# Kernel optimization log

Measured on AMD Instinct MI355X. Metric: run time of the kernel, lower is better.

Reference implementation:

```python
import jax, jax.numpy as jnp
import numpy as np
import math

N = 50000      # nodes
E = 800000     # edges
F_IN = 64      # input node features
H = 4          # heads
C = 32         # hidden_channels (per-head dim)
HC = H * C     # 128
ED = 4         # edge_dim
G = 1000       # graphs in batch


def _lin(key, fin, fout, bias=True):
    k1, k2 = jax.random.split(key)
    w = jax.random.normal(k1, (fin, fout), jnp.float32) * (1.0 / math.sqrt(fin))
    if bias:
        b = jax.random.normal(k2, (fout,), jnp.float32) * 0.02
        return w, b
    return w


def setup_inputs() -> dict:
    key = jax.random.key(0)
    ks = jax.random.split(key, 24)
    x = jax.random.normal(ks[0], (N, F_IN), jnp.float32)
    edge_index = jax.random.randint(ks[1], (2, E), 0, N)
    edge_attr = jax.random.normal(ks[2], (E, ED), jnp.float32)
    batch = jnp.sort(jax.random.randint(ks[3], (N,), 0, G))
    inp = {"x": x, "edge_index": edge_index, "edge_attr": edge_attr, "batch": batch}
    fins = [F_IN, HC, HC]
    i = 4
    for l in range(3):
        fin = fins[l]
        inp[f"wq{l+1}"], inp[f"bq{l+1}"] = _lin(ks[i], fin, HC); i += 1
        inp[f"wk{l+1}"], inp[f"bk{l+1}"] = _lin(ks[i], fin, HC); i += 1
        inp[f"wv{l+1}"], inp[f"bv{l+1}"] = _lin(ks[i], fin, HC); i += 1
        inp[f"we{l+1}"] = _lin(ks[i], ED, HC, bias=False); i += 1
        inp[f"ws{l+1}"], inp[f"bs{l+1}"] = _lin(ks[i], fin, HC); i += 1
    inp["wlin"], inp["blin"] = _lin(ks[i], HC, 1)
    return inp


def _segment_softmax(alpha, seg, n):
    # numerically-stable softmax over edges grouped by destination node
    m = jax.ops.segment_max(alpha, seg, num_segments=n)
    m = jnp.where(jnp.isfinite(m), m, 0.0)
    a = jnp.exp(alpha - m[seg])
    s = jax.ops.segment_sum(a, seg, num_segments=n)
    return a / (s[seg] + 1e-16)


def _conv(x, src, dst, ea, wq, bq, wk, bk, wv, bv, we, ws, bs):
    # PyG TransformerConv (concat=True, root_weight=True, beta=False)
    n = x.shape[0]
    q = (x @ wq + bq).reshape(n, H, C)
    k = (x @ wk + bk).reshape(n, H, C)
    v = (x @ wv + bv).reshape(n, H, C)
    e = (ea @ we).reshape(-1, H, C)          # [E,H,C] edge projection
    kj = k[src] + e                           # key of source + edge
    alpha = jnp.einsum('ehc,ehc->eh', q[dst], kj) / math.sqrt(C)  # [E,H]
    alpha = _segment_softmax(alpha, dst, n)
    msg = (v[src] + e) * alpha[..., None]     # [E,H,C]
    out = jax.ops.segment_sum(msg, dst, num_segments=n).reshape(n, HC)
    return out + x @ ws + bs                  # skip connection


def reference(x, edge_index, edge_attr, batch,
              wq1, bq1, wk1, bk1, wv1, bv1, we1, ws1, bs1,
              wq2, bq2, wk2, bk2, wv2, bv2, we2, ws2, bs2,
              wq3, bq3, wk3, bk3, wv3, bv3, we3, ws3, bs3,
              wlin, blin):
    src, dst = edge_index[0], edge_index[1]
    h = jax.nn.relu(_conv(x, src, dst, edge_attr, wq1, bq1, wk1, bk1, wv1, bv1, we1, ws1, bs1))
    h = jax.nn.relu(_conv(h, src, dst, edge_attr, wq2, bq2, wk2, bk2, wv2, bv2, we2, ws2, bs2))
    h = _conv(h, src, dst, edge_attr, wq3, bq3, wk3, bk3, wv3, bv3, we3, ws3, bs3)
    # global_mean_pool
    s = jax.ops.segment_sum(h, batch, num_segments=G)
    cnt = jax.ops.segment_sum(jnp.ones((h.shape[0],), h.dtype), batch, num_segments=G)
    pooled = s / jnp.maximum(cnt, 1.0)[:, None]
    # dropout is identity in eval mode
    return pooled @ wlin + blin
```

## Files before the change

kernel.cpp:

```cpp
#include <hip/hip_runtime.h>
#include <math.h>

#define NN 50000
#define EE 800000
#define GG 1000

typedef __attribute__((ext_vector_type(2))) _Float16 h2f;
typedef __attribute__((ext_vector_type(4))) _Float16 h4f;
typedef __attribute__((ext_vector_type(8))) _Float16 h8f;
typedef __attribute__((ext_vector_type(4))) float f32x4;

#if __has_builtin(__builtin_amdgcn_fdot2)
#define FDOT2(a, b, c) __builtin_amdgcn_fdot2((a), (b), (c), false)
#else
#define FDOT2(a, b, c) ((float)(a)[0] * (float)(b)[0] + (float)(a)[1] * (float)(b)[1] + (c))
#endif

static inline int ceil_div(int a, int b) { return (a + b - 1) / b; }

union EU { int2 i; h4f h; };


__global__ __launch_bounds__(256) void hist_k(const int* __restrict__ ei, int* __restrict__ cnt)
{
    int e = blockIdx.x * 256 + threadIdx.x;
    if (e >= EE) return;
    atomicAdd(&cnt[ei[EE + e]], 1);
}

__global__ __launch_bounds__(1024) void scan1_k(const int* __restrict__ cnt, int n,
                                                int* __restrict__ rowptr, int* __restrict__ bsum)
{
    __shared__ int tmp[1024];
    const int tid = threadIdx.x;
    const int i = blockIdx.x * 1024 + tid;
    tmp[tid] = (i < n) ? cnt[i] : 0;
    __syncthreads();
    for (int off = 1; off < 1024; off <<= 1) {
        int t = (tid >= off) ? tmp[tid - off] : 0;
        __syncthreads();
        tmp[tid] += t;
        __syncthreads();
    }
    if (i < n) rowptr[i + 1] = tmp[tid];
    if (tid == 1023) bsum[blockIdx.x] = tmp[1023];
}

__global__ __launch_bounds__(64) void scan2_k(int* __restrict__ bsum, int nb)
{
    const int t = threadIdx.x;
    int v = (t < nb) ? bsum[t] : 0;
    const int orig = v;
    for (int off = 1; off < 64; off <<= 1) {
        int n = __shfl_up(v, off);
        if (t >= off) v += n;
    }
    if (t < nb) bsum[t] = v - orig;
}

__global__ __launch_bounds__(1024) void scan3_k(int* __restrict__ rowptr,
                                                int* __restrict__ wcur,
                                                const int* __restrict__ bsum, int n)
{
    int i = blockIdx.x * 1024 + threadIdx.x;
    if (i < n) {
        int v = rowptr[i + 1] + bsum[blockIdx.x];
        rowptr[i + 1] = v;
        if (i + 1 < n) wcur[i + 1] = v;
    }
    if (i == 0) { rowptr[0] = 0; wcur[0] = 0; }
}

__global__ __launch_bounds__(256) void scatter_k(const int* __restrict__ ei,
                                                 const float4* __restrict__ ea,
                                                 int* __restrict__ wcur,
                                                 int4* __restrict__ edges)
{
    int e = blockIdx.x * 256 + threadIdx.x;
    if (e >= EE) return;
    int dst = ei[EE + e];
    int pos = atomicAdd(&wcur[dst], 1);
    float4 a = ea[e];
    EU u; u.h = h4f{(_Float16)a.x, (_Float16)a.y, (_Float16)a.z, (_Float16)a.w};
    edges[pos] = make_int4(ei[e], u.i.x, u.i.y, 0);
}

struct W12 { const float* w[12]; };

__global__ __launch_bounds__(64) void shuffle_w12(W12 ws, _Float16* __restrict__ out)
{
    const int m = blockIdx.y;
    const int K = (m < 4) ? 64 : 128;
    const int nblk = (K / 16) * 8;
    if (blockIdx.x >= nblk) return;
    const int s = blockIdx.x >> 3, c16 = blockIdx.x & 7;
    const int lane = threadIdx.x;
    const float* __restrict__ w = ws.w[m];
    const int kbase = s * 16 + (lane >> 4) * 4;
    const int col = c16 * 16 + (lane & 15);
    h4f h;
#pragma unroll
    for (int j = 0; j < 4; ++j) h[j] = (_Float16)w[(size_t)(kbase + j) * 128 + col];
    size_t base = (m < 4) ? (size_t)m * 64 * 128
                          : (size_t)4 * 64 * 128 + (size_t)(m - 4) * 128 * 128;
    reinterpret_cast<h4f*>(out + base)[(size_t)blockIdx.x * 64 + lane] = h;
}

template<int K, bool F32IN>
__global__ __launch_bounds__(256) void gemm_mfma(
    const void* __restrict__ xin, const _Float16* __restrict__ wshuf,
    const float* __restrict__ bq, const float* __restrict__ bk,
    const float* __restrict__ bv, const float* __restrict__ bs,
    _Float16* __restrict__ qout, _Float16* __restrict__ kout,
    _Float16* __restrict__ vout, float* __restrict__ skout)
{
    constexpr int KS = K / 16;
    constexpr int PADK = K + 8;
    __shared__ _Float16 xs[64 * PADK];
    __shared__ _Float16 wt[K * 128];
    const int t = threadIdx.x;
    const int bn = blockIdx.x * 64;
    if (F32IN) {
        const float* xf = (const float*)xin;
        constexpr int C4 = K / 4;
        for (int idx = t; idx < 64 * C4; idx += 256) {
            const int row = idx / C4, c4 = idx % C4;
            float4 val = make_float4(0.f, 0.f, 0.f, 0.f);
            if (bn + row < NN)
                val = reinterpret_cast<const float4*>(xf)[(size_t)(bn + row) * C4 + c4];
            h4f h = {(_Float16)val.x, (_Float16)val.y, (_Float16)val.z, (_Float16)val.w};
            *reinterpret_cast<h4f*>(&xs[row * PADK + c4 * 4]) = h;
        }
    } else {
        const _Float16* xh = (const _Float16*)xin;
        constexpr int CH = K / 8;
        for (int idx = t; idx < 64 * CH; idx += 256) {
            const int row = idx / CH, ch = idx % CH;
            h8f val = {0, 0, 0, 0, 0, 0, 0, 0};
            if (bn + row < NN)
                val = reinterpret_cast<const h8f*>(xh + (size_t)(bn + row) * K)[ch];
            *reinterpret_cast<h8f*>(&xs[row * PADK + ch * 8]) = val;
        }
    }
    __syncthreads();

    const int wid = t >> 6, lane = t & 63;
    const int rloc = wid * 16 + (lane & 15);
    const int ko = (lane >> 4) * 4;
    h4f b[KS];
#pragma unroll
    for (int s = 0; s < KS; ++s)
        b[s] = *reinterpret_cast<const h4f*>(&xs[rloc * PADK + s * 16 + ko]);

    const int node = bn + rloc;
    const int hcq = (lane >> 4) * 4;
    const float* bias[4] = {bq, bk, bv, bs};
    constexpr int WH4 = K * 128 / 4;

#pragma unroll
    for (int m = 0; m < 4; ++m) {
        const h4f* __restrict__ wg = reinterpret_cast<const h4f*>(wshuf + (size_t)m * K * 128);
        h4f* __restrict__ wl = reinterpret_cast<h4f*>(wt);
        for (int idx = t; idx < WH4; idx += 256) wl[idx] = wg[idx];
        __syncthreads();

        f32x4 acc[8];
#pragma unroll
        for (int c = 0; c < 8; ++c) acc[c] = {0, 0, 0, 0};
#pragma unroll
        for (int c = 0; c < 8; ++c)
#pragma unroll
            for (int s = 0; s < KS; ++s) {
                h4f af = wl[(s * 8 + c) * 64 + lane];
                acc[c] = __builtin_amdgcn_mfma_f32_16x16x16f16(af, b[s], acc[c], 0, 0, 0);
            }
        if (node < NN) {
            const float* bm = bias[m];
#pragma unroll
            for (int c = 0; c < 8; ++c) {
                const int hc = c * 16 + hcq;
                const float4 bb = *reinterpret_cast<const float4*>(&bm[hc]);
                float o0 = acc[c][0] + bb.x, o1 = acc[c][1] + bb.y;
                float o2 = acc[c][2] + bb.z, o3 = acc[c][3] + bb.w;
                if (m == 3) {
                    *reinterpret_cast<float4*>(&skout[(size_t)node * 128 + hc]) =
                        make_float4(o0, o1, o2, o3);
                } else {
                    _Float16* dst = (m == 0) ? qout : (m == 1) ? kout : vout;
                    h4f oh = {(_Float16)o0, (_Float16)o1, (_Float16)o2, (_Float16)o3};
                    *reinterpret_cast<h4f*>(&dst[(size_t)node * 128 + hc]) = oh;
                }
            }
        }
        __syncthreads();
    }
}

__global__ __launch_bounds__(256, 8) void node_agg(
    const int* __restrict__ rowptr, const int4* __restrict__ edges,
    const _Float16* __restrict__ qh, const _Float16* __restrict__ kh,
    const _Float16* __restrict__ vh, const float* __restrict__ we,
    const float* __restrict__ sk, _Float16* __restrict__ houth, int relu)
{
    __shared__ float we_s[4 * 128];
    const int t = threadIdx.x;
    if (t < 128)
        reinterpret_cast<float4*>(we_s)[t] = reinterpret_cast<const float4*>(we)[t];
    __syncthreads();
    const int node = blockIdx.x * 4 + (t >> 6);
    if (node >= NN) return;
    const int lane = t & 63;
    const int g = lane >> 4, sub = lane & 15, ch0 = sub * 8;
    const int beg = rowptr[node], end = rowptr[node + 1];
    const int deg = end - beg;

    const float sc = 0.17677669529663687f * 1.4426950408889634f;
    const h8f q8 = *reinterpret_cast<const h8f*>(&qh[(size_t)node * 128 + ch0]);
    float qf[8];
#pragma unroll
    for (int j = 0; j < 8; ++j) qf[j] = (float)q8[j] * sc;
    h2f qp[4];
#pragma unroll
    for (int i = 0; i < 4; ++i) {
        qp[i][0] = (_Float16)qf[2 * i];
        qp[i][1] = (_Float16)qf[2 * i + 1];
    }

    float qe[4];
#pragma unroll
    for (int d = 0; d < 4; ++d) {
        const float4 wa = *reinterpret_cast<const float4*>(&we_s[d * 128 + ch0]);
        const float4 wb = *reinterpret_cast<const float4*>(&we_s[d * 128 + ch0 + 4]);
        float pq = wa.x * qf[0] + wa.y * qf[1] + wa.z * qf[2] + wa.w * qf[3]
                 + wb.x * qf[4] + wb.y * qf[5] + wb.z * qf[6] + wb.w * qf[7];
        pq += __shfl_xor(pq, 1); pq += __shfl_xor(pq, 2);
        qe[d] = pq;
    }

    float m = -1e30f, s = 0.f;
    float acc[8] = {0, 0, 0, 0, 0, 0, 0, 0};
    float T[4] = {0, 0, 0, 0};

    const int nt = (deg + 3) >> 2;
    int p = beg + g;
    for (int i = 0; i < nt; ++i, p += 4) {
        const bool act = p < end;
        const int4 r = edges[act ? p : beg];
        const int4 ki = *reinterpret_cast<const int4*>(&kh[(size_t)r.x * 128 + ch0]);
        const int4 vi = *reinterpret_cast<const int4*>(&vh[(size_t)r.x * 128 + ch0]);
        float al = FDOT2(qp[0], __builtin_bit_cast(h2f, ki.x), 0.0f);
        al = FDOT2(qp[1], __builtin_bit_cast(h2f, ki.y), al);
        al = FDOT2(qp[2], __builtin_bit_cast(h2f, ki.z), al);
        al = FDOT2(qp[3], __builtin_bit_cast(h2f, ki.w), al);
        al += __shfl_xor(al, 1); al += __shfl_xor(al, 2);
        const h2f e01 = __builtin_bit_cast(h2f, r.y);
        const h2f e23 = __builtin_bit_cast(h2f, r.z);
        const float f0 = (float)e01[0], f1 = (float)e01[1];
        const float f2 = (float)e23[0], f3 = (float)e23[1];
        al += f0 * qe[0] + f1 * qe[1] + f2 * qe[2] + f3 * qe[3];
        al = act ? al : -1e30f;
        if (__any(al > m + 10.0f)) {
            const float mn = fmaxf(m, al);
            const float rr = exp2f(m - mn);
            s *= rr;
#pragma unroll
            for (int j = 0; j < 8; ++j) acc[j] *= rr;
#pragma unroll
            for (int d = 0; d < 4; ++d) T[d] *= rr;
            m = mn;
        }
        const float pe = exp2f(al - m);
        s += pe;
        const h2f v01 = __builtin_bit_cast(h2f, vi.x);
        const h2f v23 = __builtin_bit_cast(h2f, vi.y);
        const h2f v45 = __builtin_bit_cast(h2f, vi.z);
        const h2f v67 = __builtin_bit_cast(h2f, vi.w);
        acc[0] += pe * (float)v01[0]; acc[1] += pe * (float)v01[1];
        acc[2] += pe * (float)v23[0]; acc[3] += pe * (float)v23[1];
        acc[4] += pe * (float)v45[0]; acc[5] += pe * (float)v45[1];
        acc[6] += pe * (float)v67[0]; acc[7] += pe * (float)v67[1];
        T[0] += pe * f0; T[1] += pe * f1; T[2] += pe * f2; T[3] += pe * f3;
    }

#pragma unroll
    for (int off = 16; off <= 32; off <<= 1) {
        const float mo = __shfl_xor(m, off);
        const float so = __shfl_xor(s, off);
        const float mn = fmaxf(m, mo);
        const float r1 = exp2f(m - mn), r2 = exp2f(mo - mn);
        s = s * r1 + so * r2;
#pragma unroll
        for (int j = 0; j < 8; ++j) {
            const float ao = __shfl_xor(acc[j], off);
            acc[j] = acc[j] * r1 + ao * r2;
        }
#pragma unroll
        for (int d = 0; d < 4; ++d) {
            const float To = __shfl_xor(T[d], off);
            T[d] = T[d] * r1 + To * r2;
        }
        m = mn;
    }

    if (g == 0) {
        const float inv = 1.0f / (s + 1e-16f);
        float4 wa[4], wb[4];
#pragma unroll
        for (int d = 0; d < 4; ++d) {
            wa[d] = *reinterpret_cast<const float4*>(&we_s[d * 128 + ch0]);
            wb[d] = *reinterpret_cast<const float4*>(&we_s[d * 128 + ch0 + 4]);
        }
        const float4 s0 = *reinterpret_cast<const float4*>(&sk[(size_t)node * 128 + ch0]);
        const float4 s1 = *reinterpret_cast<const float4*>(&sk[(size_t)node * 128 + ch0 + 4]);
        float ov[8];
        ov[0] = (acc[0] + wa[0].x * T[0] + wa[1].x * T[1] + wa[2].x * T[2] + wa[3].x * T[3]) * inv + s0.x;
        ov[1] = (acc[1] + wa[0].y * T[0] + wa[1].y * T[1] + wa[2].y * T[2] + wa[3].y * T[3]) * inv + s0.y;
        ov[2] = (acc[2] + wa[0].z * T[0] + wa[1].z * T[1] + wa[2].z * T[2] + wa[3].z * T[3]) * inv + s0.z;
        ov[3] = (acc[3] + wa[0].w * T[0] + wa[1].w * T[1] + wa[2].w * T[2] + wa[3].w * T[3]) * inv + s0.w;
        ov[4] = (acc[4] + wb[0].x * T[0] + wb[1].x * T[1] + wb[2].x * T[2] + wb[3].x * T[3]) * inv + s1.x;
        ov[5] = (acc[5] + wb[0].y * T[0] + wb[1].y * T[1] + wb[2].y * T[2] + wb[3].y * T[3]) * inv + s1.y;
        ov[6] = (acc[6] + wb[0].z * T[0] + wb[1].z * T[1] + wb[2].z * T[2] + wb[3].z * T[3]) * inv + s1.z;
        ov[7] = (acc[7] + wb[0].w * T[0] + wb[1].w * T[1] + wb[2].w * T[2] + wb[3].w * T[3]) * inv + s1.w;
        h8f oh;
#pragma unroll
        for (int j = 0; j < 8; ++j) {
            float v = relu ? fmaxf(ov[j], 0.f) : ov[j];
            oh[j] = (_Float16)v;
        }
        *reinterpret_cast<h8f*>(&houth[(size_t)node * 128 + ch0]) = oh;
    }
}


__global__ __launch_bounds__(256) void boundaries_k(const int* __restrict__ batch,
                                                    int* __restrict__ gptr)
{
    int i = blockIdx.x * 256 + threadIdx.x;
    if (i >= NN) return;
    int b = batch[i];
    int bp = (i == 0) ? -1 : batch[i - 1];
    for (int g = bp + 1; g <= b; ++g) gptr[g] = i;
    if (i == NN - 1) for (int g = b + 1; g <= GG; ++g) gptr[g] = NN;
}

__global__ __launch_bounds__(128) void head_k(
    const _Float16* __restrict__ h, const int* __restrict__ gptr,
    const float* __restrict__ wlin, const float* __restrict__ blin,
    float* __restrict__ out)
{
    __shared__ float red[128];
    const int g = blockIdx.x;
    const int t = threadIdx.x;
    const int beg = gptr[g], end = gptr[g + 1];
    float p = 0.f;
    for (int n = beg; n < end; ++n) p += (float)h[(size_t)n * 128 + t];
    p *= wlin[t];
    red[t] = p;
    __syncthreads();
    for (int off = 64; off; off >>= 1) {
        if (t < off) red[t] += red[t + off];
        __syncthreads();
    }
    if (t == 0) out[g] = red[0] / fmaxf((float)(end - beg), 1.0f) + blin[0];
}

extern "C" void kernel_launch(void* const* d_in, const int* in_sizes, int n_in,
                              void* d_out, int out_size, void* d_ws, size_t ws_size,
                              hipStream_t stream)
{
    const float* x     = (const float*)d_in[0];
    const int*   ei    = (const int*)d_in[1];
    const float* ea    = (const float*)d_in[2];
    const int*   batch = (const int*)d_in[3];
    auto W = [&](int i) { return (const float*)d_in[i]; };

    char* wsb = (char*)d_ws;
    size_t off = 0;
    auto alloc = [&](size_t bytes) { void* p = wsb + off; off += (bytes + 15) & ~15ull; return p; };

    float* sk       = (float*)alloc((size_t)NN * 128 * 4);
    int4*  edges    = (int4*)alloc((size_t)EE * 16);
    _Float16* qh    = (_Float16*)alloc((size_t)NN * 128 * 2);
    _Float16* kh    = (_Float16*)alloc((size_t)NN * 128 * 2);
    _Float16* vh    = (_Float16*)alloc((size_t)NN * 128 * 2);
    _Float16* hh    = (_Float16*)alloc((size_t)NN * 128 * 2);
    _Float16* wshuf = (_Float16*)alloc(((size_t)4 * 64 * 128 + 8 * 128 * 128) * 2);
    int* cnt    = (int*)alloc((size_t)NN * 4);
    int* rowptr = (int*)alloc((size_t)(NN + 1) * 4);
    int* wcur   = (int*)alloc((size_t)NN * 4);
    int* gptr   = (int*)alloc((size_t)(GG + 1) * 4);
    int* bsum   = (int*)alloc((size_t)64 * 4);

    hipMemsetAsync(cnt, 0, NN * sizeof(int), stream);
    hist_k<<<ceil_div(EE, 256), 256, 0, stream>>>(ei, cnt);
    const int NB = ceil_div(NN, 1024);
    scan1_k<<<NB, 1024, 0, stream>>>(cnt, NN, rowptr, bsum);
    scan2_k<<<1, 64, 0, stream>>>(bsum, NB);
    scan3_k<<<NB, 1024, 0, stream>>>(rowptr, wcur, bsum, NN);
    scatter_k<<<ceil_div(EE, 256), 256, 0, stream>>>(ei, (const float4*)ea, wcur, edges);

    boundaries_k<<<ceil_div(NN, 256), 256, 0, stream>>>(batch, gptr);

    W12 w12 = {{ W(4), W(6), W(8), W(11),
                 W(13), W(15), W(17), W(20),
                 W(22), W(24), W(26), W(29) }};
    shuffle_w12<<<dim3(64, 12), 64, 0, stream>>>(w12, wshuf);
    const size_t wsz1 = (size_t)4 * 64 * 128;
    const size_t wsz2 = (size_t)4 * 128 * 128;

    auto layer = [&](int K, const void* xin, const _Float16* wsh, int relu, int wb) {
        if (K == 64)
            gemm_mfma<64, true><<<ceil_div(NN, 64), 256, 0, stream>>>(
                xin, wsh, W(wb + 1), W(wb + 3), W(wb + 5), W(wb + 8), qh, kh, vh, sk);
        else
            gemm_mfma<128, false><<<ceil_div(NN, 64), 256, 0, stream>>>(
                xin, wsh, W(wb + 1), W(wb + 3), W(wb + 5), W(wb + 8), qh, kh, vh, sk);
        node_agg<<<ceil_div(NN, 4), 256, 0, stream>>>(
            rowptr, edges, qh, kh, vh, W(wb + 6), sk, hh, relu);
    };

    layer(64,  x,  wshuf, 1, 4);
    layer(128, hh, wshuf + wsz1, 1, 13);
    layer(128, hh, wshuf + wsz1 + wsz2, 0, 22);

    head_k<<<GG, 128, 0, stream>>>(hh, gptr, W(31), W(32), (float*)d_out);
}
```

Before: 466.4 us.

## Merge scan and boundary kernels, retile GEMM so waves split output columns

New measurement: 473.8 us. About the same (+1.6%).

```diff
diff --git a/kernel.cpp b/kernel.cpp
--- a/kernel.cpp
+++ b/kernel.cpp
@@ -29,7 +29,9 @@
 }
 
 __global__ __launch_bounds__(1024) void scan1_k(const int* __restrict__ cnt, int n,
-                                                int* __restrict__ rowptr, int* __restrict__ bsum)
+                                                int* __restrict__ rowptr, int* __restrict__ bsum,
+                                                const int* __restrict__ batch,
+                                                int* __restrict__ gptr)
 {
     __shared__ int tmp[1024];
     const int tid = threadIdx.x;
@@ -44,27 +46,31 @@
     }
     if (i < n) rowptr[i + 1] = tmp[tid];
     if (tid == 1023) bsum[blockIdx.x] = tmp[1023];
-}
-
-__global__ __launch_bounds__(64) void scan2_k(int* __restrict__ bsum, int nb)
-{
-    const int t = threadIdx.x;
-    int v = (t < nb) ? bsum[t] : 0;
-    const int orig = v;
-    for (int off = 1; off < 64; off <<= 1) {
-        int n = __shfl_up(v, off);
-        if (t >= off) v += n;
-    }
-    if (t < nb) bsum[t] = v - orig;
+    if (i < NN) {
+        int b = batch[i];
+        int bp = (i == 0) ? -1 : batch[i - 1];
+        for (int g = bp + 1; g <= b; ++g) gptr[g] = i;
+        if (i == NN - 1) for (int g = b + 1; g <= GG; ++g) gptr[g] = NN;
+    }
 }
 
 __global__ __launch_bounds__(1024) void scan3_k(int* __restrict__ rowptr,
                                                 int* __restrict__ wcur,
                                                 const int* __restrict__ bsum, int n)
 {
-    int i = blockIdx.x * 1024 + threadIdx.x;
+    __shared__ int base_s;
+    const int tid = threadIdx.x;
+    if (tid < 64) {
+        int v = (tid < (int)blockIdx.x) ? bsum[tid] : 0;
+#pragma unroll
+        for (int off = 1; off < 64; off <<= 1) v += __shfl_xor(v, off);
+        if (tid == 0) base_s = v;
+    }
+    __syncthreads();
+    const int base = base_s;
+    int i = blockIdx.x * 1024 + tid;
     if (i < n) {
-        int v = rowptr[i + 1] + bsum[blockIdx.x];
+        int v = rowptr[i + 1] + base;
         rowptr[i + 1] = v;
         if (i + 1 < n) wcur[i + 1] = v;
     }
@@ -145,17 +151,17 @@
     __syncthreads();
 
     const int wid = t >> 6, lane = t & 63;
-    const int rloc = wid * 16 + (lane & 15);
-    const int ko = (lane >> 4) * 4;
-    h4f b[KS];
-#pragma unroll
-    for (int s = 0; s < KS; ++s)
-        b[s] = *reinterpret_cast<const h4f*>(&xs[rloc * PADK + s * 16 + ko]);
-
-    const int node = bn + rloc;
-    const int hcq = (lane >> 4) * 4;
+    const int col16 = lane & 15;
+    const int kq = (lane >> 4) * 4;
+    h4f b[4][KS];
+#pragma unroll
+    for (int r = 0; r < 4; ++r)
+#pragma unroll
+        for (int s = 0; s < KS; ++s)
+            b[r][s] = *reinterpret_cast<const h4f*>(&xs[(16 * r + col16) * PADK + s * 16 + kq]);
+
     const float* bias[4] = {bq, bk, bv, bs};
-    constexpr int WH4 = K * 128 / 4;
+    constexpr int WH4 = K * 32;
 
 #pragma unroll
     for (int m = 0; m < 4; ++m) {
@@ -164,31 +170,41 @@
         for (int idx = t; idx < WH4; idx += 256) wl[idx] = wg[idx];
         __syncthreads();
 
-        f32x4 acc[8];
-#pragma unroll
-        for (int c = 0; c < 8; ++c) acc[c] = {0, 0, 0, 0};
-#pragma unroll
-        for (int c = 0; c < 8; ++c)
+        f32x4 acc[2][4];
+#pragma unroll
+        for (int cl = 0; cl < 2; ++cl)
+#pragma unroll
+            for (int r = 0; r < 4; ++r) acc[cl][r] = {0, 0, 0, 0};
+#pragma unroll
+        for (int cl = 0; cl < 2; ++cl) {
+            const int c = wid * 2 + cl;
 #pragma unroll
             for (int s = 0; s < KS; ++s) {
-                h4f af = wl[(s * 8 + c) * 64 + lane];
-                acc[c] = __builtin_amdgcn_mfma_f32_16x16x16f16(af, b[s], acc[c], 0, 0, 0);
+                const h4f af = wl[(s * 8 + c) * 64 + lane];
+#pragma unroll
+                for (int r = 0; r < 4; ++r)
+                    acc[cl][r] = __builtin_amdgcn_mfma_f32_16x16x16f16(af, b[r][s], acc[cl][r], 0, 0, 0);
             }
-        if (node < NN) {
-            const float* bm = bias[m];
-#pragma unroll
-            for (int c = 0; c < 8; ++c) {
-                const int hc = c * 16 + hcq;
-                const float4 bb = *reinterpret_cast<const float4*>(&bm[hc]);
-                float o0 = acc[c][0] + bb.x, o1 = acc[c][1] + bb.y;
-                float o2 = acc[c][2] + bb.z, o3 = acc[c][3] + bb.w;
-                if (m == 3) {
-                    *reinterpret_cast<float4*>(&skout[(size_t)node * 128 + hc]) =
-                        make_float4(o0, o1, o2, o3);
-                } else {
-                    _Float16* dst = (m == 0) ? qout : (m == 1) ? kout : vout;
-                    h4f oh = {(_Float16)o0, (_Float16)o1, (_Float16)o2, (_Float16)o3};
-                    *reinterpret_cast<h4f*>(&dst[(size_t)node * 128 + hc]) = oh;
+        }
+        const float* bm = bias[m];
+#pragma unroll
+        for (int cl = 0; cl < 2; ++cl) {
+            const int hc = (wid * 2 + cl) * 16 + kq;
+            const float4 bb = *reinterpret_cast<const float4*>(&bm[hc]);
+#pragma unroll
+            for (int r = 0; r < 4; ++r) {
+                const int node = bn + 16 * r + col16;
+                if (node < NN) {
+                    float o0 = acc[cl][r][0] + bb.x, o1 = acc[cl][r][1] + bb.y;
+                    float o2 = acc[cl][r][2] + bb.z, o3 = acc[cl][r][3] + bb.w;
+                    if (m == 3) {
+                        *reinterpret_cast<float4*>(&skout[(size_t)node * 128 + hc]) =
+                            make_float4(o0, o1, o2, o3);
+                    } else {
+                        _Float16* dst = (m == 0) ? qout : (m == 1) ? kout : vout;
+                        h4f oh = {(_Float16)o0, (_Float16)o1, (_Float16)o2, (_Float16)o3};
+                        *reinterpret_cast<h4f*>(&dst[(size_t)node * 128 + hc]) = oh;
+                    }
                 }
             }
         }
@@ -332,17 +348,6 @@
 }
 
 
-__global__ __launch_bounds__(256) void boundaries_k(const int* __restrict__ batch,
-                                                    int* __restrict__ gptr)
-{
-    int i = blockIdx.x * 256 + threadIdx.x;
-    if (i >= NN) return;
-    int b = batch[i];
-    int bp = (i == 0) ? -1 : batch[i - 1];
-    for (int g = bp + 1; g <= b; ++g) gptr[g] = i;
-    if (i == NN - 1) for (int g = b + 1; g <= GG; ++g) gptr[g] = NN;
-}
-
 __global__ __launch_bounds__(128) void head_k(
     const _Float16* __restrict__ h, const int* __restrict__ gptr,
     const float* __restrict__ wlin, const float* __restrict__ blin,
@@ -394,12 +399,9 @@
     hipMemsetAsync(cnt, 0, NN * sizeof(int), stream);
     hist_k<<<ceil_div(EE, 256), 256, 0, stream>>>(ei, cnt);
     const int NB = ceil_div(NN, 1024);
-    scan1_k<<<NB, 1024, 0, stream>>>(cnt, NN, rowptr, bsum);
-    scan2_k<<<1, 64, 0, stream>>>(bsum, NB);
+    scan1_k<<<NB, 1024, 0, stream>>>(cnt, NN, rowptr, bsum, batch, gptr);
     scan3_k<<<NB, 1024, 0, stream>>>(rowptr, wcur, bsum, NN);
     scatter_k<<<ceil_div(EE, 256), 256, 0, stream>>>(ei, (const float4*)ea, wcur, edges);
-
-    boundaries_k<<<ceil_div(NN, 256), 256, 0, stream>>>(batch, gptr);
 
     W12 w12 = {{ W(4), W(6), W(8), W(11),
                  W(13), W(15), W(17), W(20),
```
